# Optimization experiments

Hardware: AMD Instinct MI355X
Metric: run time of the kernel (lower is better)

The kernel has to match this reference:

```python
import jax, jax.numpy as jnp
import numpy as np

DIM = 768
NUM_BLOCKS = 4
BLOCK = DIM // NUM_BLOCKS
SCALE = 0.02
LAMBDA = 0.01
EPS = 1e-5


def setup_inputs() -> dict:
    key = jax.random.key(0)
    ks = jax.random.split(key, 6)
    B, H, W = 64, 32, 32
    x = jax.random.normal(ks[0], (B, DIM, H, W), dtype=jnp.float32)
    w1 = jax.random.normal(ks[1], (2, NUM_BLOCKS, BLOCK, BLOCK), dtype=jnp.float32) * SCALE
    w2 = jax.random.normal(ks[2], (2, NUM_BLOCKS, BLOCK, BLOCK), dtype=jnp.float32) * SCALE
    b1 = jax.random.normal(ks[3], (2, NUM_BLOCKS, BLOCK), dtype=jnp.float32) * SCALE
    b2 = jax.random.normal(ks[4], (2, NUM_BLOCKS, BLOCK), dtype=jnp.float32) * SCALE
    gamma = jnp.ones((DIM,), dtype=jnp.float32)
    beta = jnp.zeros((DIM,), dtype=jnp.float32)
    return {"x": x, "w1": w1, "w2": w2, "b1": b1, "b2": b2,
            "gamma": gamma, "beta": beta, "H": H, "W": W}


def _softshrink(s, lam):
    return jnp.where(s > lam, s - lam, jnp.where(s < -lam, s + lam, jnp.zeros_like(s)))


def reference(x, w1, w2, b1, b2, gamma, beta, H, W):
    B, C = x.shape[0], x.shape[1]
    nb, bs = NUM_BLOCKS, C // NUM_BLOCKS
    # (B, C, H, W) -> (B, N, C)
    xt = x.reshape(B, C, H * W).transpose(0, 2, 1)
    residual = xt
    # LayerNorm over channel dim
    mu = jnp.mean(xt, axis=-1, keepdims=True)
    var = jnp.mean(jnp.square(xt - mu), axis=-1, keepdims=True)
    xn = (xt - mu) / jnp.sqrt(var + EPS) * gamma + beta
    # (B, N, nb, bs), FFT2 over (N, nb)
    xf = jnp.fft.fft2(xn.reshape(B, H * W, nb, bs), axes=(1, 2), norm='ortho')
    xr, xi = xf.real, xf.imag

    def mul(u, w):
        return jnp.einsum('bnqd,qdk->bnqk', u, w)  # block-diagonal matmul

    r1 = jax.nn.relu(mul(xr, w1[0]) - mul(xi, w1[1]) + b1[0])
    i1 = jax.nn.relu(mul(xr, w1[1]) + mul(xi, w1[0]) + b1[1])
    r2 = mul(r1, w2[0]) - mul(i1, w2[1]) + b2[0]
    i2 = mul(r1, w2[1]) + mul(i1, w2[0]) + b2[1]
    s = jnp.stack([r2, i2], axis=-1)
    s = _softshrink(s, LAMBDA)
    xc = jax.lax.complex(s[..., 0], s[..., 1])
    y = jnp.fft.ifft2(xc, axes=(1, 2), norm='ortho').real  # cast complex->real keeps real part
    y = y.reshape(B, H * W, C) + residual
    return y.transpose(0, 2, 1).reshape(B, C, H, W)
```

## Files before the change

kernel.cpp:

```cpp
#include <hip/hip_runtime.h>
#include <math.h>

#define BB 64
#define CC 768
#define NN 1024
#define BS 192
#define EPS 1e-5f
#define LAM 0.01f

typedef float  f32x4  __attribute__((ext_vector_type(4)));
typedef short  bf16x8 __attribute__((ext_vector_type(8)));

__device__ inline unsigned f2bf(float x) {
    unsigned u = __float_as_uint(x);
    u += 0x7fff + ((u >> 16) & 1);
    return u >> 16;
}
__device__ inline unsigned pack2(float r, float i) { return f2bf(r) | (f2bf(i) << 16); }
__device__ inline float bflo(unsigned v) { return __uint_as_float(v << 16); }
__device__ inline float bfhi(unsigned v) { return __uint_as_float(v & 0xffff0000u); }

__device__ inline int swz(int i) { return i ^ (((i >> 4) & 3) << 2); }

__global__ __launch_bounds__(512) void ln_stats(const float* __restrict__ x,
                                                float* __restrict__ mu,
                                                float* __restrict__ rstd) {
    int tn = threadIdx.x & 63, tc = threadIdx.x >> 6;
    int n = blockIdx.x * 256 + tn * 4, b = blockIdx.y;
    const float* xp = x + (size_t)b * CC * NN + n;
    f32x4 s = (f32x4)0.f, ss = (f32x4)0.f;
    #pragma unroll 4
    for (int c = tc; c < CC; c += 8) {
        f32x4 v = *(const f32x4*)(xp + (size_t)c * NN);
        s += v; ss += v * v;
    }
    __shared__ f32x4 sm[8][64], sq[8][64];
    sm[tc][tn] = s; sq[tc][tn] = ss;
    __syncthreads();
    if (tc == 0) {
        f32x4 S  = sm[0][tn], SS = sq[0][tn];
        #pragma unroll
        for (int i = 1; i < 8; i++) { S += sm[i][tn]; SS += sq[i][tn]; }
        f32x4 m = S * (1.f / 768.f);
        f32x4 r;
        #pragma unroll
        for (int i = 0; i < 4; i++) {
            float var = SS[i] * (1.f / 768.f) - m[i] * m[i];
            r[i] = rsqrtf(var + EPS);
        }
        *(f32x4*)(mu + (size_t)b * NN + n)   = m;
        *(f32x4*)(rstd + (size_t)b * NN + n) = r;
    }
}

__global__ void fwd_fft(const float* __restrict__ x,
                        const float* __restrict__ mu_, const float* __restrict__ rs_,
                        const float* __restrict__ gamma, const float* __restrict__ beta,
                        unsigned* __restrict__ Xp) {
    __shared__ float2 bufs[4][1024];
    int d = blockIdx.x, b = blockIdx.y, tid = threadIdx.x;

    const float* mp = mu_ + b * NN;
    const float* rp = rs_ + b * NN;
    #pragma unroll
    for (int q = 0; q < 4; q++) {
        int c = q * BS + d;
        float g = gamma[c], be = beta[c];
        const float* xp = x + ((size_t)b * CC + c) * NN;
        #pragma unroll
        for (int k = 0; k < 4; k++) {
            int n = tid + 256 * k;
            float v = (xp[n] - mp[n]) * rp[n] * g + be;
            bufs[q][swz(n)] = make_float2(v, 0.f);
        }
    }
    __syncthreads();

    #pragma unroll
    for (int sL = 0; sL < 4; sL++) {
        const int L = 256 >> (2 * sL);
        int j = tid & (L - 1);
        int base = ((tid - j) << 2) + j;
        float s1, c1;
        __sincosf(-(float)M_PI * 0.5f * (float)j / (float)L, &s1, &c1);
        float c2 = c1 * c1 - s1 * s1, s2 = 2.f * c1 * s1;
        float c3 = c2 * c1 - s2 * s1, s3 = c2 * s1 + s2 * c1;
        #pragma unroll
        for (int q = 0; q < 4; q++) {
            float2 a  = bufs[q][swz(base)];
            float2 bb = bufs[q][swz(base + L)];
            float2 cc = bufs[q][swz(base + 2 * L)];
            float2 dd = bufs[q][swz(base + 3 * L)];
            float t0r = a.x + cc.x, t0i = a.y + cc.y;
            float t1r = a.x - cc.x, t1i = a.y - cc.y;
            float t2r = bb.x + dd.x, t2i = bb.y + dd.y;
            float t3r = bb.x - dd.x, t3i = bb.y - dd.y;
            float X0r = t0r + t2r, X0i = t0i + t2i;
            float X2r = t0r - t2r, X2i = t0i - t2i;
            float X1r = t1r + t3i, X1i = t1i - t3r;
            float X3r = t1r - t3i, X3i = t1i + t3r;
            bufs[q][swz(base)]         = make_float2(X0r, X0i);
            bufs[q][swz(base + L)]     = make_float2(X1r * c1 - X1i * s1, X1r * s1 + X1i * c1);
            bufs[q][swz(base + 2 * L)] = make_float2(X2r * c2 - X2i * s2, X2r * s2 + X2i * c2);
            bufs[q][swz(base + 3 * L)] = make_float2(X3r * c3 - X3i * s3, X3r * s3 + X3i * c3);
        }
        __syncthreads();
    }

    float Xr[4][4], Xi[4][4];
    int i0 = swz(4 * tid);
    #pragma unroll
    for (int q = 0; q < 4; q++) {
        const float4* p = (const float4*)&bufs[q][i0];
        float4 u0 = p[0], u1 = p[1];
        float t0r = u0.x + u1.x, t0i = u0.y + u1.y;
        float t1r = u0.x - u1.x, t1i = u0.y - u1.y;
        float t2r = u0.z + u1.z, t2i = u0.w + u1.w;
        float t3r = u0.z - u1.z, t3i = u0.w - u1.w;
        Xr[q][0] = t0r + t2r; Xi[q][0] = t0i + t2i;
        Xr[q][1] = t1r + t3i; Xi[q][1] = t1i - t3r;
        Xr[q][2] = t0r - t2r; Xi[q][2] = t0i - t2i;
        Xr[q][3] = t1r - t3i; Xi[q][3] = t1i + t3r;
    }
    const float sc = 1.f / 64.f;
    unsigned o0[4], o1[4], o2[4], o3[4];
    #pragma unroll
    for (int m = 0; m < 4; m++) {
        float x0r = Xr[0][m], x0i = Xi[0][m];
        float x1r = Xr[1][m], x1i = Xi[1][m];
        float x2r = Xr[2][m], x2i = Xi[2][m];
        float x3r = Xr[3][m], x3i = Xi[3][m];
        float X0r = x0r + x1r + x2r + x3r, X0i = x0i + x1i + x2i + x3i;
        float X2r = x0r - x1r + x2r - x3r, X2i = x0i - x1i + x2i - x3i;
        float X1r = x0r + x1i - x2r - x3i, X1i = x0i - x1r - x2i + x3r;
        float X3r = x0r - x1i - x2r + x3i, X3i = x0i + x1r - x2i - x3r;
        o0[m] = pack2(X0r * sc, X0i * sc);
        o1[m] = pack2(X1r * sc, X1i * sc);
        o2[m] = pack2(X2r * sc, X2i * sc);
        o3[m] = pack2(X3r * sc, X3i * sc);
    }
    size_t qs = (size_t)BS * NN;
    size_t base = (((size_t)b * 4) * BS + d) * NN + 4 * tid;
    *(uint4*)(Xp + base)          = make_uint4(o0[0], o0[1], o0[2], o0[3]);
    *(uint4*)(Xp + base + qs)     = make_uint4(o1[0], o1[1], o1[2], o1[3]);
    *(uint4*)(Xp + base + 2 * qs) = make_uint4(o2[0], o2[1], o2[2], o2[3]);
    *(uint4*)(Xp + base + 3 * qs) = make_uint4(o3[0], o3[1], o3[2], o3[3]);
}

__global__ void pack_b(const float* __restrict__ w, unsigned* __restrict__ Bp) {
    int ch = blockIdx.x, q = blockIdx.y;
    const float* wr = w + (size_t)q * BS * BS;
    const float* wi = w + (size_t)(4 + q) * BS * BS;
    size_t base = ((size_t)q * 12 + ch) * (384 * 16);
    for (int r = 0; r < 24; r++) {
        int idx = r * 256 + threadIdx.x;
        int j = idx >> 4, dd = idx & 15;
        int h = j >> 1;
        int dg = ch * 16 + dd;
        float Wr = wr[(size_t)dg * BS + h];
        float Wi = wi[(size_t)dg * BS + h];
        Bp[base + idx] = (j & 1) ? pack2(Wi, Wr) : pack2(Wr, -Wi);
    }
}

__global__ __launch_bounds__(512) void fused_mlp(const unsigned* __restrict__ Ap,
                                                 const unsigned* __restrict__ Bp1,
                                                 const unsigned* __restrict__ Bp2,
                                                 const float* __restrict__ b1,
                                                 const float* __restrict__ b2,
                                                 unsigned* __restrict__ Yp) {
    __shared__ unsigned hl[192 * 68];

    const int mblk = blockIdx.x;
    const int bq   = blockIdx.y;
    const int q    = bq & 3;
    const int tid  = threadIdx.x;
    const int wave = tid >> 6;
    const int lane = tid & 63;
    const int l15  = lane & 15;
    const int quad = lane >> 4;
    const int jw   = wave * 48;

    const unsigned* a_lane = Ap + ((size_t)bq * BS + quad * 4) * NN + mblk * 64 + l15;
    const size_t bstride = 384 * 16;
    const unsigned* b1_lane = Bp1 + (size_t)q * 12 * bstride + (jw + l15) * 16 + quad * 4;
    const unsigned* b2_lane = Bp2 + (size_t)q * 12 * bstride + (jw + l15) * 16 + quad * 4;

    f32x4 acc[3][4];
    #pragma unroll
    for (int i = 0; i < 3; i++)
        #pragma unroll
        for (int j = 0; j < 4; j++)
            acc[i][j] = (f32x4)0.f;

    for (int ch = 0; ch < 12; ch++) {
        const unsigned* ap = a_lane + (size_t)(ch * 16) * NN;
        const unsigned* bp = b1_lane + ch * bstride;
        bf16x8 af[4], bfr[3];
        #pragma unroll
        for (int tm = 0; tm < 4; tm++) {
            union { unsigned u[4]; bf16x8 v; } au;
            #pragma unroll
            for (int g = 0; g < 4; g++)
                au.u[g] = ap[(size_t)g * NN + tm * 16];
            af[tm] = au.v;
        }
        #pragma unroll
        for (int tn = 0; tn < 3; tn++) {
            union { uint4 u4; bf16x8 v; } bu;
            bu.u4 = *(const uint4*)(bp + tn * 256);
            bfr[tn] = bu.v;
        }
        #pragma unroll
        for (int tn = 0; tn < 3; tn++)
            #pragma unroll
            for (int tm = 0; tm < 4; tm++)
                acc[tn][tm] = __builtin_amdgcn_mfma_f32_16x16x32_bf16(bfr[tn], af[tm], acc[tn][tm], 0, 0, 0);
    }

    #pragma unroll
    for (int tn = 0; tn < 3; tn++) {
        int hg = wave * 24 + tn * 8 + quad * 2;
        float b0r = b1[q * BS + hg];
        float b0i = b1[768 + q * BS + hg];
        float b1r_ = b1[q * BS + hg + 1];
        float b1i_ = b1[768 + q * BS + hg + 1];
        #pragma unroll
        for (int tm = 0; tm < 4; tm++) {
            int c = tm * 16 + l15;
            f32x4 a = acc[tn][tm];
            float v0 = fmaxf(a[0] + b0r, 0.f);
            float v1 = fmaxf(a[1] + b0i, 0.f);
            float v2 = fmaxf(a[2] + b1r_, 0.f);
            float v3 = fmaxf(a[3] + b1i_, 0.f);
            hl[hg * 68 + c]       = pack2(v0, v1);
            hl[(hg + 1) * 68 + c] = pack2(v2, v3);
            acc[tn][tm] = (f32x4)0.f;
        }
    }
    __syncthreads();

    for (int ch = 0; ch < 12; ch++) {
        const unsigned* bp = b2_lane + ch * bstride;
        bf16x8 af[4], bfr[3];
        #pragma unroll
        for (int tm = 0; tm < 4; tm++) {
            union { unsigned u[4]; bf16x8 v; } au;
            #pragma unroll
            for (int g = 0; g < 4; g++)
                au.u[g] = hl[(ch * 16 + quad * 4 + g) * 68 + tm * 16 + l15];
            af[tm] = au.v;
        }
        #pragma unroll
        for (int tn = 0; tn < 3; tn++) {
            union { uint4 u4; bf16x8 v; } bu;
            bu.u4 = *(const uint4*)(bp + tn * 256);
            bfr[tn] = bu.v;
        }
        #pragma unroll
        for (int tn = 0; tn < 3; tn++)
            #pragma unroll
            for (int tm = 0; tm < 4; tm++)
                acc[tn][tm] = __builtin_amdgcn_mfma_f32_16x16x32_bf16(bfr[tn], af[tm], acc[tn][tm], 0, 0, 0);
    }

    #pragma unroll
    for (int tn = 0; tn < 3; tn++) {
        int hg = wave * 24 + tn * 8 + quad * 2;
        float b0r = b2[q * BS + hg];
        float b0i = b2[768 + q * BS + hg];
        float b1r_ = b2[q * BS + hg + 1];
        float b1i_ = b2[768 + q * BS + hg + 1];
        size_t row0 = ((size_t)bq * BS + hg) * NN + mblk * 64;
        #pragma unroll
        for (int tm = 0; tm < 4; tm++) {
            int mcol = tm * 16 + l15;
            f32x4 a = acc[tn][tm];
            float v0 = a[0] + b0r, v1 = a[1] + b0i;
            float v2 = a[2] + b1r_, v3 = a[3] + b1i_;
            v0 = (v0 > LAM) ? (v0 - LAM) : ((v0 < -LAM) ? (v0 + LAM) : 0.f);
            v1 = (v1 > LAM) ? (v1 - LAM) : ((v1 < -LAM) ? (v1 + LAM) : 0.f);
            v2 = (v2 > LAM) ? (v2 - LAM) : ((v2 < -LAM) ? (v2 + LAM) : 0.f);
            v3 = (v3 > LAM) ? (v3 - LAM) : ((v3 < -LAM) ? (v3 + LAM) : 0.f);
            Yp[row0 + mcol]      = pack2(v0, v1);
            Yp[row0 + NN + mcol] = pack2(v2, v3);
        }
    }
}

__global__ void inv_fft(const float* __restrict__ x,
                        const unsigned* __restrict__ Yp,
                        float* __restrict__ out) {
    __shared__ float2 bufs[4][1024];
    int d = blockIdx.x, b = blockIdx.y, tid = threadIdx.x;

    float Ar[4][4], Ai[4][4];
    size_t qs = (size_t)BS * NN;
    size_t rowb = (((size_t)b * 4) * BS + d) * NN + 4 * tid;
    #pragma unroll
    for (int q = 0; q < 4; q++) {
        uint4 v = *(const uint4*)(Yp + rowb + (size_t)q * qs);
        Ar[q][0] = bflo(v.x); Ai[q][0] = bfhi(v.x);
        Ar[q][1] = bflo(v.y); Ai[q][1] = bfhi(v.y);
        Ar[q][2] = bflo(v.z); Ai[q][2] = bfhi(v.z);
        Ar[q][3] = bflo(v.w); Ai[q][3] = bfhi(v.w);
    }
    #pragma unroll
    for (int m = 0; m < 4; m++) {
        float x0r = Ar[0][m], x0i = Ai[0][m];
        float x1r = Ar[1][m], x1i = Ai[1][m];
        float x2r = Ar[2][m], x2i = Ai[2][m];
        float x3r = Ar[3][m], x3i = Ai[3][m];
        float Y0r = x0r + x1r + x2r + x3r, Y0i = x0i + x1i + x2i + x3i;
        float Y2r = x0r - x1r + x2r - x3r, Y2i = x0i - x1i + x2i - x3i;
        float Y1r = x0r - x1i - x2r + x3i, Y1i = x0i + x1r - x2i - x3r;
        float Y3r = x0r + x1i - x2r - x3i, Y3i = x0i - x1r - x2i + x3r;
        Ar[0][m] = Y0r; Ai[0][m] = Y0i;
        Ar[1][m] = Y1r; Ai[1][m] = Y1i;
        Ar[2][m] = Y2r; Ai[2][m] = Y2i;
        Ar[3][m] = Y3r; Ai[3][m] = Y3i;
    }
    int i0 = swz(4 * tid);
    #pragma unroll
    for (int q = 0; q < 4; q++) {
        float t0r = Ar[q][0] + Ar[q][2], t0i = Ai[q][0] + Ai[q][2];
        float t1r = Ar[q][0] - Ar[q][2], t1i = Ai[q][0] - Ai[q][2];
        float t2r = Ar[q][1] + Ar[q][3], t2i = Ai[q][1] + Ai[q][3];
        float t3r = Ar[q][1] - Ar[q][3], t3i = Ai[q][1] - Ai[q][3];
        float4* p = (float4*)&bufs[q][i0];
        p[0] = make_float4(t0r + t2r, t0i + t2i, t1r - t3i, t1i + t3r);
        p[1] = make_float4(t0r - t2r, t0i - t2i, t1r + t3i, t1i - t3r);
    }
    __syncthreads();

    #pragma unroll
    for (int sL = 0; sL < 4; sL++) {
        const int L = 4 << (2 * sL);
        int j = tid & (L - 1);
        int base = ((tid - j) << 2) + j;
        float s1, c1;
        __sincosf((float)M_PI * 0.5f * (float)j / (float)L, &s1, &c1);
        float c2 = c1 * c1 - s1 * s1, s2 = 2.f * c1 * s1;
        float c3 = c2 * c1 - s2 * s1, s3 = c2 * s1 + s2 * c1;
        #pragma unroll
        for (int q = 0; q < 4; q++) {
            float2 y0 = bufs[q][swz(base)];
            float2 y1 = bufs[q][swz(base + L)];
            float2 y2 = bufs[q][swz(base + 2 * L)];
            float2 y3 = bufs[q][swz(base + 3 * L)];
            float A1r = y1.x * c1 - y1.y * s1, A1i = y1.x * s1 + y1.y * c1;
            float A2r = y2.x * c2 - y2.y * s2, A2i = y2.x * s2 + y2.y * c2;
            float A3r = y3.x * c3 - y3.y * s3, A3i = y3.x * s3 + y3.y * c3;
            float t0r = y0.x + A2r, t0i = y0.y + A2i;
            float t1r = y0.x - A2r, t1i = y0.y - A2i;
            float t2r = A1r + A3r, t2i = A1i + A3i;
            float t3r = A1r - A3r, t3i = A1i - A3i;
            bufs[q][swz(base)]         = make_float2(t0r + t2r, t0i + t2i);
            bufs[q][swz(base + L)]     = make_float2(t1r - t3i, t1i + t3r);
            bufs[q][swz(base + 2 * L)] = make_float2(t0r - t2r, t0i - t2i);
            bufs[q][swz(base + 3 * L)] = make_float2(t1r + t3i, t1i - t3r);
        }
        __syncthreads();
    }

    const float sc = 1.f / 64.f;
    #pragma unroll
    for (int q = 0; q < 4; q++) {
        size_t row = (((size_t)b * 4 + q) * BS + d) * NN;
        const float* xp = x + row;
        #pragma unroll
        for (int k = 0; k < 4; k++) {
            int n = tid + 256 * k;
            out[row + n] = bufs[q][swz(n)].x * sc + xp[n];
        }
    }
}

extern "C" void kernel_launch(void* const* d_in, const int* in_sizes, int n_in,
                              void* d_out, int out_size, void* d_ws, size_t ws_size,
                              hipStream_t stream) {
    const float* x     = (const float*)d_in[0];
    const float* w1    = (const float*)d_in[1];
    const float* w2    = (const float*)d_in[2];
    const float* b1    = (const float*)d_in[3];
    const float* b2    = (const float*)d_in[4];
    const float* gamma = (const float*)d_in[5];
    const float* beta  = (const float*)d_in[6];

    unsigned* Xp = (unsigned*)d_ws;
    float* mu    = (float*)d_ws + (size_t)BB * CC * NN;
    float* rstd  = mu + (size_t)BB * NN;
    unsigned* Bp1 = (unsigned*)(rstd + (size_t)BB * NN);
    unsigned* Bp2 = Bp1 + (size_t)4 * 12 * 384 * 16;
    unsigned* Yp = Xp;

    pack_b<<<dim3(12, 4), 256, 0, stream>>>(w1, Bp1);
    pack_b<<<dim3(12, 4), 256, 0, stream>>>(w2, Bp2);
    ln_stats<<<dim3(NN / 256, BB), 512, 0, stream>>>(x, mu, rstd);
    fwd_fft<<<dim3(BS, BB), 256, 0, stream>>>(x, mu, rstd, gamma, beta, Xp);
    fused_mlp<<<dim3(16, 256), 512, 0, stream>>>(Xp, Bp1, Bp2, b1, b2, Yp);
    inv_fft<<<dim3(BS, BB), 256, 0, stream>>>(x, Yp, (float*)d_out);
}
```

Measured before the change: 751.2 us.

## Fuse first/last FFT stages into load/store and double-buffer MLP operand loads

The forward FFT's first radix-4 stage is now computed in registers while loading the normalized input, and the inverse FFT's last stage is folded into the output write with the residual add. This removes one LDS round trip and one barrier per FFT. The MLP kernel's two GEMM loops are software-pipelined with register double-buffering of the A and B fragments. The hidden buffer in LDS changes from 68-column padding to an XOR swizzle, which shrinks shared memory use while still avoiding bank conflicts. The cost is higher register pressure from the double buffers.

```diff
diff --git a/kernel.cpp b/kernel.cpp
--- a/kernel.cpp
+++ b/kernel.cpp
@@ -21,6 +21,10 @@
 __device__ inline float bfhi(unsigned v) { return __uint_as_float(v & 0xffff0000u); }
 
 __device__ inline int swz(int i) { return i ^ (((i >> 4) & 3) << 2); }
+
+__device__ inline int hidx(int row, int col) {
+    return row * 64 + (col ^ (((row >> 1) & 3) << 3));
+}
 
 __global__ __launch_bounds__(512) void ln_stats(const float* __restrict__ x,
                                                 float* __restrict__ mu,
@@ -60,6 +64,11 @@
     __shared__ float2 bufs[4][1024];
     int d = blockIdx.x, b = blockIdx.y, tid = threadIdx.x;
 
+    float s1f, c1f;
+    __sincosf(-(float)M_PI * 0.5f * (float)tid / 256.f, &s1f, &c1f);
+    float c2f = c1f * c1f - s1f * s1f, s2f = 2.f * c1f * s1f;
+    float c3f = c2f * c1f - s2f * s1f, s3f = c2f * s1f + s2f * c1f;
+
     const float* mp = mu_ + b * NN;
     const float* rp = rs_ + b * NN;
     #pragma unroll
@@ -67,18 +76,21 @@
         int c = q * BS + d;
         float g = gamma[c], be = beta[c];
         const float* xp = x + ((size_t)b * CC + c) * NN;
-        #pragma unroll
-        for (int k = 0; k < 4; k++) {
-            int n = tid + 256 * k;
-            float v = (xp[n] - mp[n]) * rp[n] * g + be;
-            bufs[q][swz(n)] = make_float2(v, 0.f);
-        }
+        float v0 = (xp[tid]       - mp[tid])       * rp[tid]       * g + be;
+        float v1 = (xp[tid + 256] - mp[tid + 256]) * rp[tid + 256] * g + be;
+        float v2 = (xp[tid + 512] - mp[tid + 512]) * rp[tid + 512] * g + be;
+        float v3 = (xp[tid + 768] - mp[tid + 768]) * rp[tid + 768] * g + be;
+        float t0 = v0 + v2, t1 = v0 - v2, t2 = v1 + v3, t3 = v1 - v3;
+        bufs[q][swz(tid)]       = make_float2(t0 + t2, 0.f);
+        bufs[q][swz(tid + 256)] = make_float2(t1 * c1f + t3 * s1f, t1 * s1f - t3 * c1f);
+        bufs[q][swz(tid + 512)] = make_float2((t0 - t2) * c2f, (t0 - t2) * s2f);
+        bufs[q][swz(tid + 768)] = make_float2(t1 * c3f - t3 * s3f, t1 * s3f + t3 * c3f);
     }
     __syncthreads();
 
     #pragma unroll
-    for (int sL = 0; sL < 4; sL++) {
-        const int L = 256 >> (2 * sL);
+    for (int sL = 0; sL < 3; sL++) {
+        const int L = 64 >> (2 * sL);
         int j = tid & (L - 1);
         int base = ((tid - j) << 2) + j;
         float s1, c1;
@@ -169,7 +181,7 @@
                                                  const float* __restrict__ b1,
                                                  const float* __restrict__ b2,
                                                  unsigned* __restrict__ Yp) {
-    __shared__ unsigned hl[192 * 68];
+    __shared__ unsigned hl[192 * 64];
 
     const int mblk = blockIdx.x;
     const int bq   = blockIdx.y;
@@ -193,10 +205,8 @@
         for (int j = 0; j < 4; j++)
             acc[i][j] = (f32x4)0.f;
 
-    for (int ch = 0; ch < 12; ch++) {
+    auto LOAD_A1 = [&](bf16x8 (&af)[4], int ch) {
         const unsigned* ap = a_lane + (size_t)(ch * 16) * NN;
-        const unsigned* bp = b1_lane + ch * bstride;
-        bf16x8 af[4], bfr[3];
         #pragma unroll
         for (int tm = 0; tm < 4; tm++) {
             union { unsigned u[4]; bf16x8 v; } au;
@@ -205,17 +215,43 @@
                 au.u[g] = ap[(size_t)g * NN + tm * 16];
             af[tm] = au.v;
         }
+    };
+    auto LOAD_B = [&](bf16x8 (&bfr)[3], const unsigned* blane, int ch) {
+        const unsigned* bp = blane + ch * bstride;
         #pragma unroll
         for (int tn = 0; tn < 3; tn++) {
             union { uint4 u4; bf16x8 v; } bu;
             bu.u4 = *(const uint4*)(bp + tn * 256);
             bfr[tn] = bu.v;
         }
+    };
+    auto LOAD_A2 = [&](bf16x8 (&af)[4], int ch) {
+        #pragma unroll
+        for (int tm = 0; tm < 4; tm++) {
+            union { unsigned u[4]; bf16x8 v; } au;
+            #pragma unroll
+            for (int g = 0; g < 4; g++)
+                au.u[g] = hl[hidx(ch * 16 + quad * 4 + g, tm * 16 + l15)];
+            af[tm] = au.v;
+        }
+    };
+    auto MFMA = [&](bf16x8 (&bfr)[3], bf16x8 (&af)[4]) {
         #pragma unroll
         for (int tn = 0; tn < 3; tn++)
             #pragma unroll
             for (int tm = 0; tm < 4; tm++)
                 acc[tn][tm] = __builtin_amdgcn_mfma_f32_16x16x32_bf16(bfr[tn], af[tm], acc[tn][tm], 0, 0, 0);
+    };
+
+    bf16x8 afA[4], afB[4], bfA[3], bfB[3];
+
+    LOAD_A1(afA, 0); LOAD_B(bfA, b1_lane, 0);
+    #pragma unroll
+    for (int ch = 0; ch < 12; ch += 2) {
+        LOAD_A1(afB, ch + 1); LOAD_B(bfB, b1_lane, ch + 1);
+        MFMA(bfA, afA);
+        if (ch + 2 < 12) { LOAD_A1(afA, ch + 2); LOAD_B(bfA, b1_lane, ch + 2); }
+        MFMA(bfB, afB);
     }
 
     #pragma unroll
@@ -233,35 +269,20 @@
             float v1 = fmaxf(a[1] + b0i, 0.f);
             float v2 = fmaxf(a[2] + b1r_, 0.f);
             float v3 = fmaxf(a[3] + b1i_, 0.f);
-            hl[hg * 68 + c]       = pack2(v0, v1);
-            hl[(hg + 1) * 68 + c] = pack2(v2, v3);
+            hl[hidx(hg, c)]     = pack2(v0, v1);
+            hl[hidx(hg + 1, c)] = pack2(v2, v3);
             acc[tn][tm] = (f32x4)0.f;
         }
     }
     __syncthreads();
 
-    for (int ch = 0; ch < 12; ch++) {
-        const unsigned* bp = b2_lane + ch * bstride;
-        bf16x8 af[4], bfr[3];
-        #pragma unroll
-        for (int tm = 0; tm < 4; tm++) {
-            union { unsigned u[4]; bf16x8 v; } au;
-            #pragma unroll
-            for (int g = 0; g < 4; g++)
-                au.u[g] = hl[(ch * 16 + quad * 4 + g) * 68 + tm * 16 + l15];
-            af[tm] = au.v;
-        }
-        #pragma unroll
-        for (int tn = 0; tn < 3; tn++) {
-            union { uint4 u4; bf16x8 v; } bu;
-            bu.u4 = *(const uint4*)(bp + tn * 256);
-            bfr[tn] = bu.v;
-        }
-        #pragma unroll
-        for (int tn = 0; tn < 3; tn++)
-            #pragma unroll
-            for (int tm = 0; tm < 4; tm++)
-                acc[tn][tm] = __builtin_amdgcn_mfma_f32_16x16x32_bf16(bfr[tn], af[tm], acc[tn][tm], 0, 0, 0);
+    LOAD_A2(afA, 0); LOAD_B(bfA, b2_lane, 0);
+    #pragma unroll
+    for (int ch = 0; ch < 12; ch += 2) {
+        LOAD_A2(afB, ch + 1); LOAD_B(bfB, b2_lane, ch + 1);
+        MFMA(bfA, afA);
+        if (ch + 2 < 12) { LOAD_A2(afA, ch + 2); LOAD_B(bfA, b2_lane, ch + 2); }
+        MFMA(bfB, afB);
     }
 
     #pragma unroll
@@ -334,7 +355,7 @@
     __syncthreads();
 
     #pragma unroll
-    for (int sL = 0; sL < 4; sL++) {
+    for (int sL = 0; sL < 3; sL++) {
         const int L = 4 << (2 * sL);
         int j = tid & (L - 1);
         int base = ((tid - j) << 2) + j;
@@ -363,16 +384,30 @@
         __syncthreads();
     }
 
+    float s1f, c1f;
+    __sincosf((float)M_PI * 0.5f * (float)tid / 256.f, &s1f, &c1f);
+    float c2f = c1f * c1f - s1f * s1f, s2f = 2.f * c1f * s1f;
+    float c3f = c2f * c1f - s2f * s1f, s3f = c2f * s1f + s2f * c1f;
     const float sc = 1.f / 64.f;
     #pragma unroll
     for (int q = 0; q < 4; q++) {
+        float2 y0 = bufs[q][swz(tid)];
+        float2 y1 = bufs[q][swz(tid + 256)];
+        float2 y2 = bufs[q][swz(tid + 512)];
+        float2 y3 = bufs[q][swz(tid + 768)];
+        float A1r = y1.x * c1f - y1.y * s1f, A1i = y1.x * s1f + y1.y * c1f;
+        float A2r = y2.x * c2f - y2.y * s2f;
+        float A3r = y3.x * c3f - y3.y * s3f, A3i = y3.x * s3f + y3.y * c3f;
+        float t0r = y0.x + A2r;
+        float t1r = y0.x - A2r;
+        float t2r = A1r + A3r;
+        float t3i = A1i - A3i;
         size_t row = (((size_t)b * 4 + q) * BS + d) * NN;
         const float* xp = x + row;
-        #pragma unroll
-        for (int k = 0; k < 4; k++) {
-            int n = tid + 256 * k;
-            out[row + n] = bufs[q][swz(n)].x * sc + xp[n];
-        }
+        out[row + tid]       = (t0r + t2r) * sc + xp[tid];
+        out[row + tid + 256] = (t1r - t3i) * sc + xp[tid + 256];
+        out[row + tid + 512] = (t0r - t2r) * sc + xp[tid + 512];
+        out[row + tid + 768] = (t1r + t3i) * sc + xp[tid + 768];
     }
 }
 
```

New measurement: 846.8 us. 12.7% more time.
